# Kernel optimization log

Measured on AMD Instinct MI355X. Metric: run time of the kernel, lower is better.

The kernel has to match this reference:

```python
import math
import jax, jax.numpy as jnp
import numpy as np

EMBED_DIM = 1024
NUM_HEADS = 16
HEAD_DIM = EMBED_DIM // NUM_HEADS


def setup_inputs() -> dict:
    key = jax.random.key(0)
    kx, kqkv, kproj = jax.random.split(key, 3)
    b, sq, h = 2, 2048, EMBED_DIM
    x = jax.random.normal(kx, (b, sq, h), dtype=jnp.float32)
    # torch Linear weights are [out_features, in_features]
    # xavier_uniform for qkv: bound = sqrt(6/(fan_in+fan_out))
    bound_qkv = math.sqrt(6.0 / (h + 3 * h))
    Wqkv = jax.random.uniform(kqkv, (3 * h, h), dtype=jnp.float32,
                              minval=-bound_qkv, maxval=bound_qkv)
    # kaiming_uniform(a=sqrt(5)) for proj: bound = 1/sqrt(fan_in)
    bound_p = 1.0 / math.sqrt(h)
    Wproj = jax.random.uniform(kproj, (h, h), dtype=jnp.float32,
                               minval=-bound_p, maxval=bound_p)
    bproj = jnp.zeros((h,), dtype=jnp.float32)
    # self-attention: query == key == value (module asserts equality)
    return {"query": x, "key": x, "value": x,
            "Wqkv": Wqkv, "Wproj": Wproj, "bproj": bproj}


def reference(query, key, value, Wqkv, Wproj, bproj):
    b, sq, h = query.shape
    nh, hn = NUM_HEADS, HEAD_DIM
    # permute to [sq, b, h] then flatten tokens (seq-major)
    x = jnp.transpose(query, (1, 0, 2)).reshape(sq * b, h)
    qkv = x @ Wqkv.T                       # [sq*b, 3h] (no qkv bias: add_bias_kv=False)
    qkv = qkv.reshape(sq, b, nh, 3 * hn)
    q, k, v = jnp.split(qkv, 3, axis=-1)   # each [sq, b, nh, hn]
    # view to (sq, b*nh, hn) then transpose(0,1) -> [b*nh, sq, hn] (b-major, nh-minor)
    q = q.reshape(sq, b * nh, hn).transpose(1, 0, 2)
    k = k.reshape(sq, b * nh, hn).transpose(1, 0, 2)
    v = v.reshape(sq, b * nh, hn).transpose(1, 0, 2)
    scale = 1.0 / math.sqrt(hn)
    scores = jnp.einsum('nqd,nkd->nqk', q, k) * scale   # [b*nh, sq, sq] full matrix
    attn = jax.nn.softmax(scores, axis=-1)
    ctx = jnp.einsum('nqk,nkd->nqd', attn, v)           # [b*nh, sq, hn]
    # NOTE: original code views the b*nh (b-major) dim as (nh, b) -- reproduce exactly
    ctx = ctx.reshape(nh, b, sq, hn)
    ctx = jnp.transpose(ctx, (2, 1, 0, 3)).reshape(sq * b, h)
    out = ctx @ Wproj.T + bproj
    out = out.reshape(sq, b, h)
    return jnp.transpose(out, (1, 0, 2))   # [b, sq, h]
```

## Files before the change

kernel.cpp:

```cpp
#include <hip/hip_runtime.h>
#include <stdint.h>

#define B_   2
#define SQ   2048
#define H    1024
#define NH   16
#define HN   64
#define T_TOK 4096
#define N3H  3072

typedef __bf16 bf16x8 __attribute__((ext_vector_type(8)));
typedef float  f32x4  __attribute__((ext_vector_type(4)));
typedef float  f32x16 __attribute__((ext_vector_type(16)));

#define MFMA16(a, b, c) __builtin_amdgcn_mfma_f32_16x16x32_bf16((a), (b), (c), 0, 0, 0)
#define MFMA32(a, b, c) __builtin_amdgcn_mfma_f32_32x32x16_bf16((a), (b), (c), 0, 0, 0)

#define LGKM_DRAIN() do { \
  __builtin_amdgcn_s_waitcnt(0xC07F); \
  __builtin_amdgcn_wave_barrier(); \
} while (0)

__device__ __forceinline__ uint16_t f2bf_u(float f) {
  union { float f; uint32_t u; } v; v.f = f;
  uint32_t u = v.u;
  u += 0x7fffu + ((u >> 16) & 1u);
  return (uint16_t)(u >> 16);
}

__device__ __forceinline__ uint32_t pk2(float a, float b) {
  union { __bf16 h[2]; uint32_t u; } r;
  r.h[0] = (__bf16)a;
  r.h[1] = (__bf16)b;
  return r.u;
}

__device__ __forceinline__ bf16x8 ldb8(const uint16_t* p) {
  return *reinterpret_cast<const bf16x8*>(p);
}

__device__ __forceinline__ void gll16(const uint16_t* g, uint16_t* l) {
  __builtin_amdgcn_global_load_lds(
      (const __attribute__((address_space(1))) uint32_t*)g,
      (__attribute__((address_space(3))) uint32_t*)l, 16, 0, 0);
}

__global__ __launch_bounds__(256) void convert_kernel(
    const float* __restrict__ x, const float* __restrict__ wqkv,
    const float* __restrict__ wproj,
    uint16_t* __restrict__ xb, uint16_t* __restrict__ wqkvb,
    uint16_t* __restrict__ wprojb) {
  const int XT4 = (T_TOK * H) / 4;
  const int WQ4 = (N3H * H) / 4;
  int i4 = blockIdx.x * 256 + threadIdx.x;
  const float* src;
  uint16_t* dst;
  if (i4 < XT4) {
    int i = i4 * 4;
    int t = i >> 10, c = i & 1023;
    int bi = t & 1, s = t >> 1;
    src = x + (bi * SQ + s) * H + c;
    dst = xb + i;
  } else if (i4 < XT4 + WQ4) {
    int j = (i4 - XT4) * 4;
    src = wqkv + j; dst = wqkvb + j;
  } else {
    int j = (i4 - XT4 - WQ4) * 4;
    src = wproj + j; dst = wprojb + j;
  }
  float4 v = *(const float4*)src;
  ushort4 o;
  o.x = f2bf_u(v.x); o.y = f2bf_u(v.y); o.z = f2bf_u(v.z); o.w = f2bf_u(v.w);
  *(ushort4*)dst = o;
}

__global__ __launch_bounds__(256) void gemm_qkv_kernel(
    const uint16_t* __restrict__ xb, const uint16_t* __restrict__ wb,
    uint16_t* __restrict__ Qb, uint16_t* __restrict__ Kb,
    uint16_t* __restrict__ Vtb) {
  const int lane = threadIdx.x & 63;
  const int wave = threadIdx.x >> 6;
  const int quad = lane >> 4, l16 = lane & 15;
  const int wm = wave >> 1, wn = wave & 1;
  const int row0 = blockIdx.y * 128, col0 = blockIdx.x * 128;

  __shared__ __align__(16) char smem[4 * 64 * 76 * 2];
  uint16_t* sA = (uint16_t*)smem;
  uint16_t* sB = (uint16_t*)(smem + 8192);
  uint16_t* W  = (uint16_t*)(smem) + wave * (64 * 76);

  const int lrow = lane >> 2;
  const int lk   = (lane & 3) * 8;

  f32x4 acc[4][4];
#pragma unroll
  for (int i = 0; i < 4; ++i)
#pragma unroll
    for (int j = 0; j < 4; ++j) acc[i][j] = (f32x4){0.f, 0.f, 0.f, 0.f};

  for (int k0 = 0; k0 < H; k0 += 32) {
#pragma unroll
    for (int c = 0; c < 2; ++c) {
      int g = c * 4 + wave;
      gll16(xb + (size_t)(row0 + g * 16 + lrow) * H + k0 + lk, sA + g * 512);
      gll16(wb + (size_t)(col0 + g * 16 + lrow) * H + k0 + lk, sB + g * 512);
    }
    __syncthreads();
    bf16x8 af[4], bfr[4];
#pragma unroll
    for (int mt = 0; mt < 4; ++mt)
      af[mt] = ldb8(sA + (wm * 64 + mt * 16 + l16) * 32 + quad * 8);
#pragma unroll
    for (int nt = 0; nt < 4; ++nt)
      bfr[nt] = ldb8(sB + (wn * 64 + nt * 16 + l16) * 32 + quad * 8);
#pragma unroll
    for (int mt = 0; mt < 4; ++mt)
#pragma unroll
      for (int nt = 0; nt < 4; ++nt)
        acc[mt][nt] = MFMA16(af[mt], bfr[nt], acc[mt][nt]);
    __syncthreads();
  }

  const int c0 = col0 + wn * 64;
  const int cm = c0 >> 6;
  const int hd = cm / 3;
  const int which = cm - hd * 3;
  const int t0 = row0 + wm * 64;

  if (which < 2) {
    const float qs = (which == 0) ? 0.18033688f : 1.0f;
#pragma unroll
    for (int mt = 0; mt < 4; ++mt)
#pragma unroll
      for (int nt = 0; nt < 4; ++nt)
#pragma unroll
        for (int r = 0; r < 4; ++r)
          W[(mt * 16 + quad * 4 + r) * 76 + nt * 16 + l16] = f2bf_u(acc[mt][nt][r] * qs);
    LGKM_DRAIN();
    uint16_t* dstb = (which == 0) ? Qb : Kb;
    const int t8 = lane >> 3, d0 = (lane & 7) * 8;
#pragma unroll
    for (int it = 0; it < 8; ++it) {
      int tl = it * 8 + t8;
      int t = t0 + tl;
      int s = t >> 1;
      int n = (t & 1) * NH + hd;
      bf16x8 vv = ldb8(W + tl * 76 + d0);
      *(bf16x8*)(dstb + (size_t)(n * SQ + s) * HN + d0) = vv;
    }
  } else {
    uint32_t* W32 = (uint32_t*)W;
#pragma unroll
    for (int mt = 0; mt < 4; ++mt)
#pragma unroll
      for (int nt = 0; nt < 4; ++nt) {
        int base = (nt * 16 + l16) * 76 + mt * 8 + quad * 2;
        W32[base >> 1] =
            (uint32_t)f2bf_u(acc[mt][nt][0]) | ((uint32_t)f2bf_u(acc[mt][nt][2]) << 16);
        W32[(base >> 1) + 16] =
            (uint32_t)f2bf_u(acc[mt][nt][1]) | ((uint32_t)f2bf_u(acc[mt][nt][3]) << 16);
      }
    LGKM_DRAIN();
    const int dl = lane >> 3;
    const int bi = (lane >> 2) & 1;
    const int sc = (lane & 3) * 8;
    const int s0 = (row0 >> 1) + wm * 32;
    const int n = bi * NH + hd;
    const int sb = sc & ~15;
    const int hh = (sc >> 3) & 1;
#pragma unroll
    for (int it = 0; it < 8; ++it) {
      int d = it * 8 + dl;
      const uint16_t* Wr = W + d * 76 + bi * 32 + sb + hh * 4;
      union { uint64_t q[2]; bf16x8 v; } vv;
      vv.q[0] = *(const uint64_t*)(Wr);
      vv.q[1] = *(const uint64_t*)(Wr + 8);
      *(bf16x8*)(Vtb + (size_t)(n * HN + d) * SQ + s0 + sc) = vv.v;
    }
  }
}

__global__ __launch_bounds__(512, 4) void attn_kernel(
    const uint16_t* __restrict__ Qb, const uint16_t* __restrict__ Kb,
    const uint16_t* __restrict__ Vtb, uint16_t* __restrict__ ctxb) {
  const int lane = threadIdx.x & 63;
  const int wave = threadIdx.x >> 6;
  const int l32 = lane & 31;
  const int hi  = lane >> 5;
  const int wq = wave & 3;
  const int hf = wave >> 2;

  const int bid = blockIdx.x;
  const int xcd = bid & 7, slot = bid >> 3;
  const int head = xcd * 4 + (slot >> 4);
  const int qt   = slot & 15;
  const int q0w  = qt * 128 + wq * 32;

  const uint16_t* Qh = Qb + (size_t)head * SQ * HN;
  const uint16_t* Kh = Kb + (size_t)head * SQ * HN;
  const uint16_t* Vh = Vtb + (size_t)head * HN * SQ;

  __shared__ __align__(16) char smem[65536];
  float (*cacc)[64][33] = (float(*)[64][33])smem;

  const int lr8 = lane >> 3, lc8 = lane & 7;
  const int sc8 = (lc8 - lr8) & 7;

  bf16x8 qf[4];
#pragma unroll
  for (int dc = 0; dc < 4; ++dc)
    qf[dc] = ldb8(Qh + (size_t)(q0w + l32) * HN + dc * 16 + hi * 8);

  f32x16 acc[2];
#pragma unroll
  for (int dt = 0; dt < 2; ++dt)
#pragma unroll
    for (int e = 0; e < 16; ++e) acc[dt][e] = 0.f;
  float lrun = 0.f;

  auto STAGE = [&](int b, int kt) {
    uint16_t* sK = (uint16_t*)(smem + hf * 32768 + b * 16384);
    uint16_t* sV = sK + 4096;
    const int kbase = (hf * 16 + kt) * 64;
#pragma unroll
    for (int j = 0; j < 2; ++j) {
      int rr = wq * 16 + j * 8;
      gll16(Kh + (size_t)(kbase + rr + lr8) * HN + sc8 * 8, sK + rr * 64);
      gll16(Vh + (size_t)(rr + lr8) * SQ + kbase + sc8 * 8, sV + rr * 64);
    }
  };

  STAGE(0, 0);
  __syncthreads();

#pragma unroll 2
  for (int kt = 0; kt < 16; ++kt) {
    const int cur = kt & 1;
    if (kt < 15) STAGE(cur ^ 1, kt + 1);
    const uint16_t* sK = (const uint16_t*)(smem + hf * 32768 + cur * 16384);
    const uint16_t* sV = sK + 4096;

#pragma unroll
    for (int ktile = 0; ktile < 2; ++ktile) {
      f32x16 s;
#pragma unroll
      for (int e = 0; e < 16; ++e) s[e] = 0.f;
      __builtin_amdgcn_s_setprio(1);
#pragma unroll
      for (int dc = 0; dc < 4; ++dc) {
        bf16x8 kf = ldb8(sK + (ktile * 32 + l32) * 64 + ((dc * 2 + hi + l32) & 7) * 8);
        s = MFMA32(kf, qf[dc], s);
      }
      __builtin_amdgcn_s_setprio(0);
      uint32_t c[8];
#pragma unroll
      for (int i = 0; i < 8; ++i) {
        float p0 = __builtin_amdgcn_exp2f(s[2 * i]);
        float p1 = __builtin_amdgcn_exp2f(s[2 * i + 1]);
        lrun += p0;
        lrun += p1;
        c[i] = pk2(p0, p1);
      }
      union { uint32_t u[4]; bf16x8 v; } pa0, pa1;
#pragma unroll
      for (int x = 0; x < 4; ++x) { pa0.u[x] = c[x]; pa1.u[x] = c[4 + x]; }
      __builtin_amdgcn_s_setprio(1);
#pragma unroll
      for (int dt = 0; dt < 2; ++dt) {
        bf16x8 v0 = ldb8(sV + (dt * 32 + l32) * 64 + ((ktile * 4 + 0 + hi + l32) & 7) * 8);
        bf16x8 v1 = ldb8(sV + (dt * 32 + l32) * 64 + ((ktile * 4 + 2 + hi + l32) & 7) * 8);
        acc[dt] = MFMA32(pa0.v, v0, acc[dt]);
        acc[dt] = MFMA32(pa1.v, v1, acc[dt]);
      }
      __builtin_amdgcn_s_setprio(0);
    }
    __syncthreads();
  }

  if (hf) {
    float* dst = &cacc[wq][lane][0];
#pragma unroll
    for (int dt = 0; dt < 2; ++dt)
#pragma unroll
      for (int e = 0; e < 16; ++e) dst[dt * 16 + e] = acc[dt][e];
    dst[32] = lrun;
  }
  __syncthreads();
  if (hf) return;
  {
    const float* src = &cacc[wq][lane][0];
#pragma unroll
    for (int dt = 0; dt < 2; ++dt)
#pragma unroll
      for (int e = 0; e < 16; ++e) acc[dt][e] += src[dt * 16 + e];
    lrun += src[32];
  }

  float ls = lrun + __shfl_xor(lrun, 32);
  float rinv = __builtin_amdgcn_rcpf(ls);
  uint16_t* ctile = (uint16_t*)(smem + 36864) + wq * (32 * 72);
#pragma unroll
  for (int e = 0; e < 16; ++e) {
    int qe = (e & 3) + 8 * (e >> 2) + 4 * hi;
    float rv = __shfl(rinv, qe);
    ctile[qe * 72 + l32]      = f2bf_u(acc[0][e] * rv);
    ctile[qe * 72 + 32 + l32] = f2bf_u(acc[1][e] * rv);
  }
  LGKM_DRAIN();
  {
    const int q8 = lane >> 3, d0 = (lane & 7) * 8;
    const int gcb = (head >> 1) * HN;
#pragma unroll
    for (int it = 0; it < 4; ++it) {
      int ql = it * 8 + q8;
      bf16x8 vv = ldb8(ctile + ql * 72 + d0);
      int row = 2 * (q0w + ql) + (head & 1);
      *(bf16x8*)(ctxb + (size_t)row * H + gcb + d0) = vv;
    }
  }
}

__global__ __launch_bounds__(256) void gemm_proj_kernel(
    const uint16_t* __restrict__ ab, const uint16_t* __restrict__ wb,
    const float* __restrict__ bias, float* __restrict__ out) {
  const int lane = threadIdx.x & 63;
  const int wave = threadIdx.x >> 6;
  const int quad = lane >> 4, l16 = lane & 15;
  const int row0 = blockIdx.y * 128, col0 = blockIdx.x * 64;

  __shared__ __align__(16) uint16_t sA[128 * 32];
  __shared__ __align__(16) uint16_t sB[64 * 32];

  const int lrow = lane >> 2;
  const int lk   = (lane & 3) * 8;

  f32x4 acc[2][4];
#pragma unroll
  for (int i = 0; i < 2; ++i)
#pragma unroll
    for (int j = 0; j < 4; ++j) acc[i][j] = (f32x4){0.f, 0.f, 0.f, 0.f};

  for (int k0 = 0; k0 < H; k0 += 32) {
#pragma unroll
    for (int c = 0; c < 2; ++c) {
      int g = c * 4 + wave;
      gll16(ab + (size_t)(row0 + g * 16 + lrow) * H + k0 + lk, sA + g * 512);
    }
    gll16(wb + (size_t)(col0 + wave * 16 + lrow) * H + k0 + lk, sB + wave * 512);
    __syncthreads();
    bf16x8 af[2], bfr[4];
#pragma unroll
    for (int mt = 0; mt < 2; ++mt)
      af[mt] = ldb8(sA + (wave * 32 + mt * 16 + l16) * 32 + quad * 8);
#pragma unroll
    for (int nt = 0; nt < 4; ++nt)
      bfr[nt] = ldb8(sB + (nt * 16 + l16) * 32 + quad * 8);
#pragma unroll
    for (int mt = 0; mt < 2; ++mt)
#pragma unroll
      for (int nt = 0; nt < 4; ++nt)
        acc[mt][nt] = MFMA16(af[mt], bfr[nt], acc[mt][nt]);
    __syncthreads();
  }

#pragma unroll
  for (int mt = 0; mt < 2; ++mt)
#pragma unroll
    for (int nt = 0; nt < 4; ++nt)
#pragma unroll
      for (int r = 0; r < 4; ++r) {
        int m = row0 + wave * 32 + mt * 16 + quad * 4 + r;
        int c = col0 + nt * 16 + l16;
        int s = m >> 1, bi = m & 1;
        out[(size_t)(bi * SQ + s) * H + c] = acc[mt][nt][r] + bias[c];
      }
}

extern "C" void kernel_launch(void* const* d_in, const int* in_sizes, int n_in,
                              void* d_out, int out_size, void* d_ws, size_t ws_size,
                              hipStream_t stream) {
  const float* x     = (const float*)d_in[0];
  const float* wqkv  = (const float*)d_in[3];
  const float* wproj = (const float*)d_in[4];
  const float* bproj = (const float*)d_in[5];
  float* out = (float*)d_out;

  char* ws = (char*)d_ws;
  uint16_t* xb     = (uint16_t*)(ws);
  uint16_t* wqkvb  = (uint16_t*)(ws + (8ull  << 20));
  uint16_t* wprojb = (uint16_t*)(ws + (14ull << 20));
  uint16_t* Qb     = (uint16_t*)(ws + (16ull << 20));
  uint16_t* Kb     = (uint16_t*)(ws + (24ull << 20));
  uint16_t* Vtb    = (uint16_t*)(ws + (32ull << 20));
  uint16_t* ctxb   = (uint16_t*)(ws + (40ull << 20));

  convert_kernel<<<8192, 256, 0, stream>>>(x, wqkv, wproj, xb, wqkvb, wprojb);
  gemm_qkv_kernel<<<dim3(N3H / 128, T_TOK / 128), 256, 0, stream>>>(xb, wqkvb, Qb, Kb, Vtb);
  attn_kernel<<<512, 512, 0, stream>>>(Qb, Kb, Vtb, ctxb);
  gemm_proj_kernel<<<dim3(H / 64, T_TOK / 128), 256, 0, stream>>>(ctxb, wprojb, bproj, out);
}
```

Baseline: 210.5 us.

## Double-buffer LDS tiles in QKV and projection GEMMs with prefetch

Both GEMM kernels now use two LDS buffers and issue the global-to-LDS loads for the next K tile before computing on the current one, leaving one barrier per iteration. The goal is to hide global load latency behind the MFMA work. Wave priority is raised around the MFMA block. The QKV smem array is 38912 bytes, enough for two 16KB stages. The risk is that the single barrier may not wait for the async direct-to-LDS loads (vmcnt) before the next iteration reads them, depending on how gll16 and __syncthreads interact.

```diff
diff --git a/kernel.cpp b/kernel.cpp
--- a/kernel.cpp
+++ b/kernel.cpp
@@ -85,9 +85,7 @@
   const int row0 = blockIdx.y * 128, col0 = blockIdx.x * 128;
 
   __shared__ __align__(16) char smem[4 * 64 * 76 * 2];
-  uint16_t* sA = (uint16_t*)smem;
-  uint16_t* sB = (uint16_t*)(smem + 8192);
-  uint16_t* W  = (uint16_t*)(smem) + wave * (64 * 76);
+  uint16_t* W = (uint16_t*)(smem) + wave * (64 * 76);
 
   const int lrow = lane >> 2;
   const int lk   = (lane & 3) * 8;
@@ -98,14 +96,26 @@
 #pragma unroll
     for (int j = 0; j < 4; ++j) acc[i][j] = (f32x4){0.f, 0.f, 0.f, 0.f};
 
-  for (int k0 = 0; k0 < H; k0 += 32) {
+  auto STAGE = [&](int b, int k0) {
+    uint16_t* sA = (uint16_t*)(smem + b * 16384);
+    uint16_t* sB = sA + 4096;
 #pragma unroll
     for (int c = 0; c < 2; ++c) {
       int g = c * 4 + wave;
       gll16(xb + (size_t)(row0 + g * 16 + lrow) * H + k0 + lk, sA + g * 512);
       gll16(wb + (size_t)(col0 + g * 16 + lrow) * H + k0 + lk, sB + g * 512);
     }
-    __syncthreads();
+  };
+
+  STAGE(0, 0);
+  __syncthreads();
+
+#pragma unroll 2
+  for (int t = 0; t < 32; ++t) {
+    const int cur = t & 1;
+    if (t < 31) STAGE(cur ^ 1, (t + 1) * 32);
+    const uint16_t* sA = (const uint16_t*)(smem + cur * 16384);
+    const uint16_t* sB = sA + 4096;
     bf16x8 af[4], bfr[4];
 #pragma unroll
     for (int mt = 0; mt < 4; ++mt)
@@ -113,11 +123,13 @@
 #pragma unroll
     for (int nt = 0; nt < 4; ++nt)
       bfr[nt] = ldb8(sB + (wn * 64 + nt * 16 + l16) * 32 + quad * 8);
+    __builtin_amdgcn_s_setprio(1);
 #pragma unroll
     for (int mt = 0; mt < 4; ++mt)
 #pragma unroll
       for (int nt = 0; nt < 4; ++nt)
         acc[mt][nt] = MFMA16(af[mt], bfr[nt], acc[mt][nt]);
+    __builtin_amdgcn_s_setprio(0);
     __syncthreads();
   }
 
@@ -328,8 +340,7 @@
   const int quad = lane >> 4, l16 = lane & 15;
   const int row0 = blockIdx.y * 128, col0 = blockIdx.x * 64;
 
-  __shared__ __align__(16) uint16_t sA[128 * 32];
-  __shared__ __align__(16) uint16_t sB[64 * 32];
+  __shared__ __align__(16) char smem[2 * 12288];
 
   const int lrow = lane >> 2;
   const int lk   = (lane & 3) * 8;
@@ -340,14 +351,26 @@
 #pragma unroll
     for (int j = 0; j < 4; ++j) acc[i][j] = (f32x4){0.f, 0.f, 0.f, 0.f};
 
-  for (int k0 = 0; k0 < H; k0 += 32) {
+  auto STAGE = [&](int b, int k0) {
+    uint16_t* sA = (uint16_t*)(smem + b * 12288);
+    uint16_t* sB = sA + 4096;
 #pragma unroll
     for (int c = 0; c < 2; ++c) {
       int g = c * 4 + wave;
       gll16(ab + (size_t)(row0 + g * 16 + lrow) * H + k0 + lk, sA + g * 512);
     }
     gll16(wb + (size_t)(col0 + wave * 16 + lrow) * H + k0 + lk, sB + wave * 512);
-    __syncthreads();
+  };
+
+  STAGE(0, 0);
+  __syncthreads();
+
+#pragma unroll 2
+  for (int t = 0; t < 32; ++t) {
+    const int cur = t & 1;
+    if (t < 31) STAGE(cur ^ 1, (t + 1) * 32);
+    const uint16_t* sA = (const uint16_t*)(smem + cur * 12288);
+    const uint16_t* sB = sA + 4096;
     bf16x8 af[2], bfr[4];
 #pragma unroll
     for (int mt = 0; mt < 2; ++mt)
@@ -355,11 +378,13 @@
 #pragma unroll
     for (int nt = 0; nt < 4; ++nt)
       bfr[nt] = ldb8(sB + (nt * 16 + l16) * 32 + quad * 8);
+    __builtin_amdgcn_s_setprio(1);
 #pragma unroll
     for (int mt = 0; mt < 2; ++mt)
 #pragma unroll
       for (int nt = 0; nt < 4; ++nt)
         acc[mt][nt] = MFMA16(af[mt], bfr[nt], acc[mt][nt]);
+    __builtin_amdgcn_s_setprio(0);
     __syncthreads();
   }
 
```

Measured after the change: 201.6 us. 1.04x faster.
